# Performance work log

Hardware: AMD Instinct MI355X
Metric: run time of the kernel (lower is better)

Reference implementation:

```python
import jax, jax.numpy as jnp
import numpy as np

# Static configuration matching the selected code path:
#   mode='inject_subject', is_self_attn=True, layer_id='up_blocks.0' (inject layer, bank hit)
#   alpha = AlphaScheduler.alpha(step=20, total=50, 'up_blocks.0') = 0.8 * 0.6 = 0.48
B, L, D, H = 4, 1024, 1280, 20
DH = D // H  # 64
ALPHA = 0.48


def setup_inputs() -> dict:
    key = jax.random.key(0)
    ks = jax.random.split(key, 8)
    w = lambda k, shp: (jax.random.normal(k, shp, dtype=jnp.float32) * 0.02)
    return {
        "hidden_states": jax.random.normal(ks[0], (B, L, D), dtype=jnp.float32),
        "Wq": w(ks[1], (D, D)),
        "Wk": w(ks[2], (D, D)),
        "Wv": w(ks[3], (D, D)),
        "Wo": w(ks[4], (D, D)),
        "bo": jnp.zeros((D,), dtype=jnp.float32),
        # cached background K/V, stored after head_to_batch_dim -> [B*H, L_bg, DH]
        "K_bg": jax.random.normal(ks[5], (B * H, L, DH), dtype=jnp.float32),
        "V_bg": jax.random.normal(ks[6], (B * H, L, DH), dtype=jnp.float32),
    }


def _head_to_batch(x):  # [B, L, D] -> [B*H, L, DH]
    b, l, _ = x.shape
    return x.reshape(b, l, H, DH).transpose(0, 2, 1, 3).reshape(b * H, l, DH)


def _batch_to_head(x):  # [B*H, L, DH] -> [B, L, D]
    bh, l, _ = x.shape
    b = bh // H
    return x.reshape(b, H, l, DH).transpose(0, 2, 1, 3).reshape(b, l, D)


def reference(hidden_states, Wq, Wk, Wv, Wo, bo, K_bg, V_bg):
    # q/k/v projections (self-attention: k, v from hidden_states)
    q = _head_to_batch(hidden_states @ Wq)  # [B*H, L, DH]
    k = _head_to_batch(hidden_states @ Wk)
    v = _head_to_batch(hidden_states @ Wv)

    # inject_subject: concat cached background K/V scaled by alpha along kv-seq dim
    k = jnp.concatenate([k, ALPHA * K_bg], axis=1)  # [B*H, 2L, DH]
    v = jnp.concatenate([v, ALPHA * V_bg], axis=1)

    # _sdpa: q scaled by scale*sqrt(dh), SDPA divides by sqrt(dh) -> net factor `scale`
    scale = 1.0 / jnp.sqrt(jnp.asarray(DH, dtype=q.dtype))
    scores = jnp.einsum('bqd,bkd->bqk', q, k) * scale  # [B*H, L, 2L]
    probs = jax.nn.softmax(scores, axis=-1)
    context = jnp.einsum('bqk,bkd->bqd', probs, v)  # [B*H, L, DH]

    out = _batch_to_head(context) @ Wo + bo  # to_out[0] linear
    return out
```

## Files before the change

kernel.cpp:

```cpp
#include <hip/hip_runtime.h>
#include <hip/hip_bf16.h>

#define B_   4
#define L_   1024
#define D_   1280
#define H_   20
#define DH_  64
#define BH_  (B_*H_)
#define L2_  (2*L_)
#define ALPHA_ 0.48f
#define QSCALE_ 0.180336880f

typedef __attribute__((ext_vector_type(8))) short short8;
typedef __attribute__((ext_vector_type(4))) float float4v;

__device__ __forceinline__ float exp2_fast(float x) {
    float r;
    asm volatile("v_exp_f32 %0, %1" : "=v"(r) : "v"(x));
    return r;
}

__device__ __forceinline__ ushort f2bf(float f) {
    union { float f; unsigned int i; } v; v.f = f;
    unsigned int i = v.i;
    unsigned int r = i + 0x7FFF + ((i >> 16) & 1);
    return (ushort)(r >> 16);
}
__device__ __forceinline__ short8 pack8(float4 f0, float4 f1) {
    short8 o;
    o[0] = (short)f2bf(f0.x); o[1] = (short)f2bf(f0.y);
    o[2] = (short)f2bf(f0.z); o[3] = (short)f2bf(f0.w);
    o[4] = (short)f2bf(f1.x); o[5] = (short)f2bf(f1.y);
    o[6] = (short)f2bf(f1.z); o[7] = (short)f2bf(f1.w);
    return o;
}
__device__ __forceinline__ void pack4_store(ushort* dst, float a, float b, float c, float d) {
    union { __hip_bfloat162 h; unsigned int u; } x, y;
    x.h = __float22bfloat162_rn(make_float2(a, b));
    y.h = __float22bfloat162_rn(make_float2(c, d));
    uint2 v; v.x = x.u; v.y = y.u;
    *(uint2*)dst = v;
}

__device__ __forceinline__ void async16(const void* g, void* l) {
    __builtin_amdgcn_global_load_lds(
        (__attribute__((address_space(1))) void*)g,
        (__attribute__((address_space(3))) void*)l, 16, 0, 0);
}

__global__ __launch_bounds__(256) void prep(
    const float* __restrict__ w0, const float* __restrict__ w1,
    const float* __restrict__ w2, const float* __restrict__ w3,
    ushort* __restrict__ Wt,
    const float* __restrict__ Vbg, ushort* __restrict__ Vt,
    const float* __restrict__ X, ushort* __restrict__ Xb,
    const float* __restrict__ Kbg, ushort* __restrict__ Kcv) {
    int bi = blockIdx.x, tid = threadIdx.x;
    __shared__ __align__(16) ushort t[64 * 72];
    if (bi < 2880) {
        bool doScale = (bi >= 1600);
        const float* src; int srcld; long sbase;
        ushort* dst = nullptr; int dstld = 0; long dbase = 0;
        ushort* vout = nullptr;
        if (bi < 1600) {
            int z = bi / 400, t4 = bi % 400;
            int by = t4 / 20, bx = t4 % 20;
            const float* srcs[4] = {w0, w1, w2, w3};
            src = srcs[z]; srcld = D_; dstld = D_;
            sbase = (long)(by * 64) * D_ + bx * 64;
            dst = Wt + (long)z * D_ * D_;
            dbase = (long)(bx * 64) * D_ + by * 64;
        } else {
            int j = bi - 1600;
            int bh = j >> 4, kt = j & 15;
            src = Vbg; srcld = DH_;
            sbase = ((long)bh * L_ + kt * 64) * DH_;
            vout = Vt + (((long)bh * 32 + 16 + kt) << 12);
        }
        int ldr = tid >> 3, ldc = (tid & 7) * 8;
#pragma unroll
        for (int i = 0; i < 2; i++) {
            int y = ldr + 32 * i;
            long idx = sbase + (long)y * srcld + ldc;
            float4 f0 = *(const float4*)&src[idx];
            float4 f1 = *(const float4*)&src[idx + 4];
            if (doScale) {
                f0.x *= ALPHA_; f0.y *= ALPHA_; f0.z *= ALPHA_; f0.w *= ALPHA_;
                f1.x *= ALPHA_; f1.y *= ALPHA_; f1.z *= ALPHA_; f1.w *= ALPHA_;
            }
            *(short8*)&t[y * 72 + ldc] = pack8(f0, f1);
        }
        __syncthreads();
        if (bi < 1600) {
            int r8 = (tid & 7) * 8, c0 = tid >> 3;
#pragma unroll
            for (int i = 0; i < 2; i++) {
                int c = c0 + i * 32;
                short8 o;
#pragma unroll
                for (int j2 = 0; j2 < 8; j2++) o[j2] = (short)t[(r8 + j2) * 72 + c];
                *(short8*)&dst[dbase + (long)c * dstld + r8] = o;
            }
        } else {
#pragma unroll
            for (int i = 0; i < 2; i++) {
                int jj = i * 256 + tid;
                int cc = jj >> 6, d2 = jj & 63;
                int rb = (cc >> 2) * 32 + (cc & 3) * 4;
                short8 o;
#pragma unroll
                for (int e = 0; e < 8; e++)
                    o[e] = (short)t[(rb + (e >> 2) * 16 + (e & 3)) * 72 + d2];
                *(short8*)&vout[(long)jj * 8] = o;
            }
        }
    } else if (bi < 5440) {
        long i = ((long)(bi - 2880) * 256 + tid) * 8;
        *(short8*)&Xb[i] = pack8(*(const float4*)&X[i], *(const float4*)&X[i + 4]);
    } else {
        int j2 = bi - 5440;
        int bh = j2 >> 4, kt = j2 & 15;
        const float* src = Kbg + ((long)bh * L_ + kt * 64) * DH_;
#pragma unroll
        for (int i = 0; i < 2; i++) {
            int r = i * 256 + tid;
            int kv = r >> 3, cd = r & 7;
            long idx = (long)kv * 64 + cd * 8;
            *(short8*)&t[kv * 72 + cd * 8] =
                pack8(*(const float4*)&src[idx], *(const float4*)&src[idx + 4]);
        }
        __syncthreads();
        ushort* outp = Kcv + (((long)bh * 16 + kt) << 12);
#pragma unroll
        for (int i = 0; i < 2; i++) {
            int jj = i * 256 + tid;
            int c = jj >> 6, kv = jj & 63;
            *(short8*)&outp[(long)jj * 8] = *(const short8*)&t[kv * 72 + c * 8];
        }
    }
}

template<int BMt, int BNt, int WROWS, int WCOLS>
__global__ __launch_bounds__(256) void gemm_tpl(
    const ushort* __restrict__ A, const ushort* __restrict__ Bt,
    ushort* __restrict__ Qp, ushort* __restrict__ Kp, ushort* __restrict__ Vt,
    float* __restrict__ Out, const float* __restrict__ bo, int mode) {
    constexpr int MI = BMt / WROWS / 16;
    constexpr int NI = BNt / WCOLS / 16;
    constexpr int ASZ = BMt * 32, BSZ = BNt * 32;
    constexpr int RB = 1280 / BNt;
    constexpr int NLD = BMt / 64 + BNt / 64;
    __shared__ __align__(16) ushort Al[2 * ASZ];
    __shared__ __align__(16) ushort Bl[2 * BSZ];
    int tid = threadIdx.x;
    int bx = blockIdx.x, by = blockIdx.y;
    int w = tid >> 6, lane = tid & 63, l15 = lane & 15, quad = lane >> 4;
    int wm = (w / WCOLS) * (BMt / WROWS);
    int wn = (w % WCOLS) * (BNt / WCOLS);
    float4v acc[MI][NI] = {};
    const int K = 1280;
    constexpr int NK = 40;
    const ushort* Arow = A + (long)by * BMt * K + (tid >> 2) * K + (tid & 3) * 8;
    const ushort* Brow = Bt + (long)bx * BNt * K + (tid >> 2) * K + (tid & 3) * 8;

    auto stage = [&](int ki, int b) {
#pragma unroll
        for (int i = 0; i < BMt / 64; i++)
            async16(Arow + (long)i * 64 * K + ki * 32, &Al[b * ASZ + (i * 4 + w) * 512]);
#pragma unroll
        for (int i = 0; i < BNt / 64; i++)
            async16(Brow + (long)i * 64 * K + ki * 32, &Bl[b * BSZ + (i * 4 + w) * 512]);
    };

    stage(0, 0);
    for (int ki = 0; ki < NK; ki++) {
        int cur = ki & 1;
        if (ki + 1 < NK) {
            stage(ki + 1, 1 - cur);
            if constexpr (NLD == 4) asm volatile("s_waitcnt vmcnt(4)" ::: "memory");
            else if constexpr (NLD == 3) asm volatile("s_waitcnt vmcnt(3)" ::: "memory");
            else asm volatile("s_waitcnt vmcnt(0)" ::: "memory");
        } else {
            asm volatile("s_waitcnt vmcnt(0)" ::: "memory");
        }
        __builtin_amdgcn_sched_barrier(0);
        __builtin_amdgcn_s_barrier();
        __builtin_amdgcn_sched_barrier(0);
        short8 av[MI], bv[NI];
#pragma unroll
        for (int mi = 0; mi < MI; mi++)
            av[mi] = *(const short8*)&Al[cur * ASZ + (wm + mi * 16 + l15) * 32 + quad * 8];
#pragma unroll
        for (int ni = 0; ni < NI; ni++)
            bv[ni] = *(const short8*)&Bl[cur * BSZ + (wn + ni * 16 + l15) * 32 + quad * 8];
#pragma unroll
        for (int mi = 0; mi < MI; mi++)
#pragma unroll
            for (int ni = 0; ni < NI; ni++)
                acc[mi][ni] = __builtin_amdgcn_mfma_f32_16x16x32_bf16(av[mi], bv[ni], acc[mi][ni], 0, 0, 0);
        __builtin_amdgcn_sched_barrier(0);
        __builtin_amdgcn_s_barrier();
    }

    if (mode == 0) {
        int which = bx / RB;
#pragma unroll
        for (int mi = 0; mi < MI; mi++) {
            int m0 = by * BMt + wm + mi * 16 + quad * 4;
            int b = m0 >> 10, l0 = m0 & 1023;
#pragma unroll
            for (int ni = 0; ni < NI; ni++) {
                int n = bx * BNt + wn + ni * 16 + l15;
                int np = n - which * 1280;
                int h = np >> 6, dh = np & 63;
                if (which == 0) {
#pragma unroll
                    for (int r = 0; r < 4; r++)
                        Qp[((long)(b * H_ + h) * L_ + l0 + r) * DH_ + dh] =
                            f2bf(acc[mi][ni][r] * QSCALE_);
                } else if (which == 1) {
                    long kb = ((((long)(b * H_ + h) * 16 + (l0 >> 6)) * 8 + (dh >> 3)) * 64
                               + (l0 & 63)) * 8 + (dh & 7);
#pragma unroll
                    for (int r = 0; r < 4; r++)
                        Kp[kb + r * 8] = f2bf(acc[mi][ni][r]);
                } else {
                    int j = l0 & 63;
                    int cc = ((j >> 5) << 2) | ((j >> 2) & 3);
                    int eb = ((j >> 4) & 1) << 2;
                    pack4_store(&Vt[((((long)(b * H_ + h) * 32 + (l0 >> 6)) * 8
                                      + cc) * 64 + dh) * 8 + eb],
                                acc[mi][ni][0], acc[mi][ni][1],
                                acc[mi][ni][2], acc[mi][ni][3]);
                }
            }
        }
    } else {
#pragma unroll
        for (int mi = 0; mi < MI; mi++) {
            int mloc = wm + mi * 16 + quad * 4;
#pragma unroll
            for (int ni = 0; ni < NI; ni++) {
                int nloc = wn + ni * 16 + l15;
#pragma unroll
                for (int r = 0; r < 4; r++) {
                    int m = by * BMt + mloc + r;
                    int n = bx * BNt + nloc;
                    Out[(long)m * D_ + n] = acc[mi][ni][r] + bo[n];
                }
            }
        }
    }
}

__global__ __launch_bounds__(256) void flash_attn(
    const ushort* __restrict__ Qp, const ushort* __restrict__ Kp,
    const ushort* __restrict__ Kbg, const ushort* __restrict__ Vt,
    ushort* __restrict__ Ctx) {
    __shared__ __align__(16) ushort Kl[2 * 4096], Vl[2 * 4096];
    int tid = threadIdx.x;
    int w = tid >> 6, lane = tid & 63, l15 = lane & 15, quad = lane >> 4;
    int bi = blockIdx.x;
    int bh = (bi & 7) * 10 + ((bi >> 3) % 10);
    int qt = bi / 80;

    short8 aq[2];
    const ushort* Qb = Qp + ((long)bh * L_ + qt * 64 + w * 16) * DH_;
#pragma unroll
    for (int ks = 0; ks < 2; ks++)
        aq[ks] = *(const short8*)&Qb[l15 * DH_ + ks * 32 + quad * 8];

    float rs = 0.f;
    float4v O[4] = {};

    auto stage = [&](int kt, int b) {
        const ushort* Ksrc = (kt < 16)
            ? Kp  + (((long)bh * 16 + kt) << 12)
            : Kbg + (((long)bh * 16 + (kt - 16)) << 12);
        const ushort* Vsrc = Vt + (((long)bh * 32 + kt) << 12);
#pragma unroll
        for (int i = 0; i < 2; i++) {
            int c = w * 2 + i;
            async16(&Ksrc[c * 512 + lane * 8], &Kl[b * 4096 + c * 512]);
            async16(&Vsrc[c * 512 + lane * 8], &Vl[b * 4096 + c * 512]);
        }
    };

    stage(0, 0);
    for (int kt = 0; kt < 32; kt++) {
        int cur = kt & 1;
        if (kt + 1 < 32) {
            stage(kt + 1, 1 - cur);
            asm volatile("s_waitcnt vmcnt(4)" ::: "memory");
        } else {
            asm volatile("s_waitcnt vmcnt(0)" ::: "memory");
        }
        __builtin_amdgcn_sched_barrier(0);
        __builtin_amdgcn_s_barrier();
        __builtin_amdgcn_sched_barrier(0);
        bool bg = (kt >= 16);
        float4v s4[4] = {};
#pragma unroll
        for (int ks = 0; ks < 2; ks++) {
            short8 bk[4];
#pragma unroll
            for (int nt = 0; nt < 4; nt++)
                bk[nt] = *(const short8*)&Kl[cur * 4096 + (ks * 4 + quad) * 512 + (nt * 16 + l15) * 8];
#pragma unroll
            for (int nt = 0; nt < 4; nt++)
                s4[nt] = __builtin_amdgcn_mfma_f32_16x16x32_bf16(bk[nt], aq[ks], s4[nt], 0, 0, 0);
        }
        float p[4][4];
#pragma unroll
        for (int nt = 0; nt < 4; nt++)
#pragma unroll
            for (int r = 0; r < 4; r++) {
                float sv = s4[nt][r];
                if (bg) sv *= ALPHA_;
                p[nt][r] = exp2_fast(sv);
                rs += p[nt][r];
            }
        short8 ap[2];
#pragma unroll
        for (int ks = 0; ks < 2; ks++) {
            union { __hip_bfloat162 h[4]; short8 s; } u;
            u.h[0] = __float22bfloat162_rn(make_float2(p[2 * ks][0], p[2 * ks][1]));
            u.h[1] = __float22bfloat162_rn(make_float2(p[2 * ks][2], p[2 * ks][3]));
            u.h[2] = __float22bfloat162_rn(make_float2(p[2 * ks + 1][0], p[2 * ks + 1][1]));
            u.h[3] = __float22bfloat162_rn(make_float2(p[2 * ks + 1][2], p[2 * ks + 1][3]));
            ap[ks] = u.s;
        }
#pragma unroll
        for (int ks = 0; ks < 2; ks++) {
            short8 bv[4];
#pragma unroll
            for (int nt = 0; nt < 4; nt++)
                bv[nt] = *(const short8*)&Vl[cur * 4096 + (ks * 4 + quad) * 512 + (nt * 16 + l15) * 8];
#pragma unroll
            for (int nt = 0; nt < 4; nt++)
                O[nt] = __builtin_amdgcn_mfma_f32_16x16x32_bf16(bv[nt], ap[ks], O[nt], 0, 0, 0);
        }
        __builtin_amdgcn_sched_barrier(0);
        __builtin_amdgcn_s_barrier();
    }
    float v = rs;
    v += __shfl_xor(v, 16);
    v += __shfl_xor(v, 32);
    float rcp = 1.f / v;
    int b = bh / H_, h = bh % H_;
    long l = qt * 64 + w * 16 + l15;
#pragma unroll
    for (int nt = 0; nt < 4; nt++)
        pack4_store(&Ctx[(long)(b * L_ + l) * D_ + h * DH_ + nt * 16 + quad * 4],
                    O[nt][0] * rcp, O[nt][1] * rcp,
                    O[nt][2] * rcp, O[nt][3] * rcp);
}

extern "C" void kernel_launch(void* const* d_in, const int* in_sizes, int n_in,
                              void* d_out, int out_size, void* d_ws, size_t ws_size,
                              hipStream_t stream) {
    const float* X   = (const float*)d_in[0];
    const float* Wq  = (const float*)d_in[1];
    const float* Wk  = (const float*)d_in[2];
    const float* Wv  = (const float*)d_in[3];
    const float* Wo  = (const float*)d_in[4];
    const float* bo  = (const float*)d_in[5];
    const float* Kbg = (const float*)d_in[6];
    const float* Vbg = (const float*)d_in[7];

    char* ws = (char*)d_ws;
    size_t off = 0;
    auto alloc = [&](size_t bytes) {
        void* p = ws + off;
        off = (off + bytes + 255) & ~(size_t)255;
        return p;
    };
    ushort* Wt    = (ushort*)alloc((size_t)4 * D_ * D_ * 2);
    ushort* Qp    = (ushort*)alloc((size_t)BH_ * L_ * DH_ * 2);
    ushort* Kp    = (ushort*)alloc((size_t)BH_ * L_ * DH_ * 2);
    ushort* Kcv   = (ushort*)alloc((size_t)BH_ * L_ * DH_ * 2);
    ushort* Vt    = (ushort*)alloc((size_t)BH_ * DH_ * L2_ * 2);
    ushort* Xb    = (ushort*)alloc((size_t)B_ * L_ * D_ * 2);
    ushort* Ctx   = Xb;
    ushort* Wqkv_t = Wt;
    ushort* Wo_t   = Wt + (size_t)3 * D_ * D_;

    prep<<<6720, 256, 0, stream>>>(Wq, Wk, Wv, Wo, Wt, Vbg, Vt, X, Xb, Kbg, Kcv);
    gemm_tpl<128, 128, 2, 2><<<dim3(30, 32), 256, 0, stream>>>(
        Xb, Wqkv_t, Qp, Kp, Vt, nullptr, nullptr, 0);
    flash_attn<<<dim3(1280), 256, 0, stream>>>(Qp, Kp, Kcv, Vt, Ctx);
    gemm_tpl<64, 128, 1, 4><<<dim3(10, 64), 256, 0, stream>>>(
        Ctx, Wo_t, nullptr, nullptr, nullptr, (float*)d_out, bo, 1);
}
```

Baseline: 295.5 us.

## Halve flash-attention KV tile to 32 keys and retile output projection GEMM

Result: no change. 291.5 us (-1.3%).

```diff
diff --git a/kernel.cpp b/kernel.cpp
--- a/kernel.cpp
+++ b/kernel.cpp
@@ -179,6 +179,7 @@
             stage(ki + 1, 1 - cur);
             if constexpr (NLD == 4) asm volatile("s_waitcnt vmcnt(4)" ::: "memory");
             else if constexpr (NLD == 3) asm volatile("s_waitcnt vmcnt(3)" ::: "memory");
+            else if constexpr (NLD == 2) asm volatile("s_waitcnt vmcnt(2)" ::: "memory");
             else asm volatile("s_waitcnt vmcnt(0)" ::: "memory");
         } else {
             asm volatile("s_waitcnt vmcnt(0)" ::: "memory");
@@ -257,7 +258,7 @@
     const ushort* __restrict__ Qp, const ushort* __restrict__ Kp,
     const ushort* __restrict__ Kbg, const ushort* __restrict__ Vt,
     ushort* __restrict__ Ctx) {
-    __shared__ __align__(16) ushort Kl[2 * 4096], Vl[2 * 4096];
+    __shared__ __align__(16) ushort Kl[2 * 2048], Vl[2 * 2048];
     int tid = threadIdx.x;
     int w = tid >> 6, lane = tid & 63, l15 = lane & 15, quad = lane >> 4;
     int bi = blockIdx.x;
@@ -273,75 +274,62 @@
     float rs = 0.f;
     float4v O[4] = {};
 
-    auto stage = [&](int kt, int b) {
+    auto stage = [&](int it, int b) {
+        int kt = it >> 1, h32 = it & 1;
         const ushort* Ksrc = (kt < 16)
             ? Kp  + (((long)bh * 16 + kt) << 12)
             : Kbg + (((long)bh * 16 + (kt - 16)) << 12);
         const ushort* Vsrc = Vt + (((long)bh * 32 + kt) << 12);
-#pragma unroll
-        for (int i = 0; i < 2; i++) {
-            int c = w * 2 + i;
-            async16(&Ksrc[c * 512 + lane * 8], &Kl[b * 4096 + c * 512]);
-            async16(&Vsrc[c * 512 + lane * 8], &Vl[b * 4096 + c * 512]);
-        }
+        async16(&Ksrc[(w * 2 + (lane >> 5)) * 512 + h32 * 256 + (lane & 31) * 8],
+                &Kl[b * 2048 + w * 512]);
+        async16(&Vsrc[(h32 * 4 + w) * 512 + lane * 8], &Vl[b * 2048 + w * 512]);
     };
 
     stage(0, 0);
-    for (int kt = 0; kt < 32; kt++) {
-        int cur = kt & 1;
-        if (kt + 1 < 32) {
-            stage(kt + 1, 1 - cur);
-            asm volatile("s_waitcnt vmcnt(4)" ::: "memory");
-        } else {
-            asm volatile("s_waitcnt vmcnt(0)" ::: "memory");
-        }
-        __builtin_amdgcn_sched_barrier(0);
-        __builtin_amdgcn_s_barrier();
-        __builtin_amdgcn_sched_barrier(0);
-        bool bg = (kt >= 16);
-        float4v s4[4] = {};
+    __syncthreads();
+    for (int it = 0; it < 64; it++) {
+        int cur = it & 1;
+        if (it + 1 < 64) stage(it + 1, 1 - cur);
+        bool bg = (it >= 32);
+        float4v s4[2] = {};
 #pragma unroll
         for (int ks = 0; ks < 2; ks++) {
-            short8 bk[4];
-#pragma unroll
-            for (int nt = 0; nt < 4; nt++)
-                bk[nt] = *(const short8*)&Kl[cur * 4096 + (ks * 4 + quad) * 512 + (nt * 16 + l15) * 8];
-#pragma unroll
-            for (int nt = 0; nt < 4; nt++)
-                s4[nt] = __builtin_amdgcn_mfma_f32_16x16x32_bf16(bk[nt], aq[ks], s4[nt], 0, 0, 0);
-        }
-        float p[4][4];
+            short8 bk[2];
+#pragma unroll
+            for (int nt2 = 0; nt2 < 2; nt2++)
+                bk[nt2] = *(const short8*)&Kl[cur * 2048 + (ks * 4 + quad) * 256
+                                              + (nt2 * 16 + l15) * 8];
+#pragma unroll
+            for (int nt2 = 0; nt2 < 2; nt2++)
+                s4[nt2] = __builtin_amdgcn_mfma_f32_16x16x32_bf16(bk[nt2], aq[ks], s4[nt2], 0, 0, 0);
+        }
+        float p[2][4];
+#pragma unroll
+        for (int j = 0; j < 2; j++)
+#pragma unroll
+            for (int r = 0; r < 4; r++) {
+                float sv = s4[j][r];
+                if (bg) sv *= ALPHA_;
+                p[j][r] = exp2_fast(sv);
+                rs += p[j][r];
+            }
+        short8 ap;
+        {
+            union { __hip_bfloat162 h[4]; short8 s; } u;
+            u.h[0] = __float22bfloat162_rn(make_float2(p[0][0], p[0][1]));
+            u.h[1] = __float22bfloat162_rn(make_float2(p[0][2], p[0][3]));
+            u.h[2] = __float22bfloat162_rn(make_float2(p[1][0], p[1][1]));
+            u.h[3] = __float22bfloat162_rn(make_float2(p[1][2], p[1][3]));
+            ap = u.s;
+        }
+        short8 bv[4];
 #pragma unroll
         for (int nt = 0; nt < 4; nt++)
-#pragma unroll
-            for (int r = 0; r < 4; r++) {
-                float sv = s4[nt][r];
-                if (bg) sv *= ALPHA_;
-                p[nt][r] = exp2_fast(sv);
-                rs += p[nt][r];
-            }
-        short8 ap[2];
-#pragma unroll
-        for (int ks = 0; ks < 2; ks++) {
-            union { __hip_bfloat162 h[4]; short8 s; } u;
-            u.h[0] = __float22bfloat162_rn(make_float2(p[2 * ks][0], p[2 * ks][1]));
-            u.h[1] = __float22bfloat162_rn(make_float2(p[2 * ks][2], p[2 * ks][3]));
-            u.h[2] = __float22bfloat162_rn(make_float2(p[2 * ks + 1][0], p[2 * ks + 1][1]));
-            u.h[3] = __float22bfloat162_rn(make_float2(p[2 * ks + 1][2], p[2 * ks + 1][3]));
-            ap[ks] = u.s;
-        }
-#pragma unroll
-        for (int ks = 0; ks < 2; ks++) {
-            short8 bv[4];
-#pragma unroll
-            for (int nt = 0; nt < 4; nt++)
-                bv[nt] = *(const short8*)&Vl[cur * 4096 + (ks * 4 + quad) * 512 + (nt * 16 + l15) * 8];
-#pragma unroll
-            for (int nt = 0; nt < 4; nt++)
-                O[nt] = __builtin_amdgcn_mfma_f32_16x16x32_bf16(bv[nt], ap[ks], O[nt], 0, 0, 0);
-        }
-        __builtin_amdgcn_sched_barrier(0);
-        __builtin_amdgcn_s_barrier();
+            bv[nt] = *(const short8*)&Vl[cur * 2048 + quad * 512 + (nt * 16 + l15) * 8];
+#pragma unroll
+        for (int nt = 0; nt < 4; nt++)
+            O[nt] = __builtin_amdgcn_mfma_f32_16x16x32_bf16(bv[nt], ap, O[nt], 0, 0, 0);
+        __syncthreads();
     }
     float v = rs;
     v += __shfl_xor(v, 16);
@@ -389,6 +377,6 @@
     gemm_tpl<128, 128, 2, 2><<<dim3(30, 32), 256, 0, stream>>>(
         Xb, Wqkv_t, Qp, Kp, Vt, nullptr, nullptr, 0);
     flash_attn<<<dim3(1280), 256, 0, stream>>>(Qp, Kp, Kcv, Vt, Ctx);
-    gemm_tpl<64, 128, 1, 4><<<dim3(10, 64), 256, 0, stream>>>(
+    gemm_tpl<64, 64, 2, 2><<<dim3(20, 64), 256, 0, stream>>>(
         Ctx, Wo_t, nullptr, nullptr, nullptr, (float*)d_out, bo, 1);
 }
```
